# Optimization experiments

Hardware: AMD Instinct MI355X
Metric: run time of the kernel (lower is better)

Reference implementation:

```python
import jax, jax.numpy as jnp
import numpy as np

TOPK = 2


def setup_inputs() -> dict:
    key = jax.random.key(0)
    ks = jax.random.split(key, 6)
    B, S, D, H, M = 2, 2048, 256, 8, 8
    s = 0.02
    return {
        "x": jax.random.normal(ks[0], (B, S, D), jnp.float32),
        "Wq": jax.random.normal(ks[1], (D, H * D), jnp.float32) * s,
        "bq": jnp.zeros((H * D,), jnp.float32),
        "Wr": jax.random.normal(ks[2], (D, M), jnp.float32) * s,
        "br": jnp.zeros((M,), jnp.float32),
        "Wk": jax.random.normal(ks[3], (M, D, H * D), jnp.float32) * s,
        "bk": jnp.zeros((M, H * D), jnp.float32),
        "Wv": jax.random.normal(ks[4], (M, D, H * D), jnp.float32) * s,
        "bv": jnp.zeros((M, H * D), jnp.float32),
        "Wo": jax.random.normal(ks[5], (H * D, D), jnp.float32) * s,
        "bo": jnp.zeros((D,), jnp.float32),
        "bias0": jnp.zeros((B, M), jnp.float32),
    }


def reference(x, Wq, bq, Wr, br, Wk, bk, Wv, bv, Wo, bo, bias0):
    B, S, D = x.shape
    M, _, HD = Wk.shape
    H = HD // D
    # query projection and head split: [B,S,H,D] (head dim == n_text_state)
    q = (x @ Wq + bq).reshape(B, S, H, D)
    # router + aux-loss-free bias-adjusted top-k routing (DeepSeek-V3 style)
    scores = jax.nn.softmax(x @ Wr + br, axis=-1)                 # [B,S,M]
    biased = scores + bias0[:, None, :]
    _, idx = jax.lax.top_k(biased, TOPK)                          # [B,S,TOPK]
    mask = jax.nn.one_hot(idx, M, dtype=scores.dtype).sum(-2)     # [B,S,M] in {0,1}
    routing = scores * mask
    routing = routing / routing.sum(-1, keepdims=True)
    # per-memory linear-attention state: M_m = sum_s r[b,s,m] * k (x) v, fused over all memories
    k_all = (jnp.einsum('bsd,mde->mbse', x, Wk) + bk[:, None, None, :]).reshape(M, B, S, H, D)
    v_all = (jnp.einsum('bsd,mde->mbse', x, Wv) + bv[:, None, None, :]).reshape(M, B, S, H, D)
    mem = jnp.einsum('bsm,mbshk,mbshv->bhkv', routing, k_all, v_all)  # [B,H,D,D]
    # fused read-out (replaces per-timestep python loop): o[b,s,h,v] = sum_k mem[b,h,k,v] q[b,s,h,k]
    o = jnp.einsum('bhkv,bshk->bshv', mem, q)                     # [B,S,H,D]
    return o.reshape(B, S, H * D) @ Wo + bo
```

## Files before the change

kernel.cpp:

```cpp
#include <hip/hip_runtime.h>

typedef __attribute__((ext_vector_type(8))) short bf16x8;
typedef __attribute__((ext_vector_type(4))) float f32x4;

#define DEV static __device__ __forceinline__

DEV unsigned short f2bf(float f){
  union { float f; unsigned u; } v; v.f = f;
  unsigned r = v.u + 0x7fffu + ((v.u >> 16) & 1u);
  return (unsigned short)(r >> 16);
}
DEV float bf2f(unsigned short u){
  union { unsigned u; float f; } v; v.u = ((unsigned)u) << 16;
  return v.f;
}
DEV unsigned long long pk4(float a, float b, float c, float d){
  unsigned lo = (unsigned)f2bf(a) | ((unsigned)f2bf(b) << 16);
  unsigned hi = (unsigned)f2bf(c) | ((unsigned)f2bf(d) << 16);
  return ((unsigned long long)hi << 32) | lo;
}

__global__ __launch_bounds__(256) void k_prep(const float* __restrict__ x,
                                              const float* __restrict__ Wq,
                                              const float* __restrict__ Wr,
                                              const float* __restrict__ br,
                                              const float* __restrict__ Wk,
                                              const float* __restrict__ Wv,
                                              const float* __restrict__ Wo,
                                              const float* __restrict__ bias0,
                                              unsigned short* __restrict__ WkT,
                                              unsigned short* __restrict__ WvT,
                                              unsigned short* __restrict__ WoT,
                                              unsigned short* __restrict__ Wqb,
                                              unsigned short* __restrict__ xb,
                                              unsigned short* __restrict__ xT,
                                              float* __restrict__ routT){
  __shared__ float tile[32*33];
  __shared__ float lg[32][8];
  __shared__ float rt2[32][8];
  int bid = blockIdx.x;
  int t = threadIdx.x;
  int tx = t & 31, ty = t >> 5;

  if (bid < 8192){
    const float* src = (bid < 4096) ? Wk : Wv;
    unsigned short* dst = (bid < 4096) ? WkT : WvT;
    int q = bid & 4095;
    int bat = q >> 9, rem = q & 511;
    int c0 = (rem >> 3) * 32, r0 = (rem & 7) * 32;
    size_t boff = (size_t)bat * 256 * 2048;
    for (int i = 0; i < 4; i++)
      tile[(ty + i*8)*33 + tx] = src[boff + (size_t)(r0 + ty + i*8) * 2048 + c0 + tx];
    __syncthreads();
    for (int i = 0; i < 4; i++)
      dst[boff + (size_t)(c0 + ty + i*8) * 256 + r0 + tx] = f2bf(tile[tx*33 + ty + i*8]);
  } else if (bid < 8704){
    int q = bid - 8192;
    int c0 = (q >> 6) * 32, r0 = (q & 63) * 32;
    for (int i = 0; i < 4; i++)
      tile[(ty + i*8)*33 + tx] = Wo[(size_t)(r0 + ty + i*8) * 256 + c0 + tx];
    __syncthreads();
    for (int i = 0; i < 4; i++)
      WoT[(size_t)(c0 + ty + i*8) * 2048 + r0 + tx] = f2bf(tile[tx*33 + ty + i*8]);
  } else if (bid < 8960){
    int q = bid - 8704;
    size_t idx = (size_t)q * 2048 + t * 8;
    f32x4 a = *(const f32x4*)(Wq + idx);
    f32x4 b = *(const f32x4*)(Wq + idx + 4);
    *(unsigned long long*)(Wqb + idx)     = pk4(a[0], a[1], a[2], a[3]);
    *(unsigned long long*)(Wqb + idx + 4) = pk4(b[0], b[1], b[2], b[3]);
  } else if (bid < 9984){
    int q = bid - 8960;
    int bat = q >> 9, rem = q & 511;
    int c0 = (rem >> 6) * 32, r0 = (rem & 63) * 32;
    size_t boff = (size_t)bat * 2048 * 256;
    for (int i = 0; i < 4; i++){
      float v = x[boff + (size_t)(r0 + ty + i*8) * 256 + c0 + tx];
      tile[(ty + i*8)*33 + tx] = v;
      xb[boff + (size_t)(r0 + ty + i*8) * 256 + c0 + tx] = f2bf(v);
    }
    __syncthreads();
    for (int i = 0; i < 4; i++)
      xT[(size_t)(bat*256 + c0 + ty + i*8) * 2048 + r0 + tx] = f2bf(tile[tx*33 + ty + i*8]);
  } else {
    int row = t >> 3, mm = t & 7;
    int n = (bid - 9984) * 32 + row;
    const float* xr = x + (size_t)n * 256;
    float acc = 0.f;
    for (int d = 0; d < 256; d++) acc += xr[d] * Wr[d * 8 + mm];
    acc += br[mm];
    lg[row][mm] = acc;
    __syncthreads();
    if (t < 32){
      int r = t; int n2 = (bid - 9984) * 32 + r; int b = n2 >> 11;
      float mx = -1e30f;
      for (int i = 0; i < 8; i++) mx = fmaxf(mx, lg[r][i]);
      float s[8]; float sum = 0.f;
      for (int i = 0; i < 8; i++){ s[i] = __expf(lg[r][i] - mx); sum += s[i]; }
      for (int i = 0; i < 8; i++) s[i] /= sum;
      float bb[8];
      for (int i = 0; i < 8; i++) bb[i] = s[i] + bias0[b * 8 + i];
      int i1 = 0;
      for (int i = 1; i < 8; i++) if (bb[i] > bb[i1]) i1 = i;
      int i2 = -1;
      for (int i = 0; i < 8; i++){ if (i == i1) continue; if (i2 < 0 || bb[i] > bb[i2]) i2 = i; }
      float wsum = s[i1] + s[i2];
      for (int i = 0; i < 8; i++)
        rt2[r][i] = (i == i1) ? s[i1] / wsum : ((i == i2) ? s[i2] / wsum : 0.f);
    }
    __syncthreads();
    int n3 = (bid - 9984) * 32 + row;
    int b = n3 >> 11, sl = n3 & 2047;
    routT[((size_t)b * 8 + mm) * 2048 + sl] = rt2[row][mm];
  }
}

__global__ __launch_bounds__(256) void k_usum(const unsigned short* __restrict__ xb,
                                              const float* __restrict__ routT,
                                              float* __restrict__ upart, float* __restrict__ rhop){
  __shared__ float rl[128];
  int bid = blockIdx.x;
  int sc = bid & 15, bm = bid >> 4, b = bm >> 3;
  int t = threadIdx.x;
  int s0 = sc * 128;
  if (t < 128) rl[t] = routT[(size_t)bm * 2048 + s0 + t];
  __syncthreads();
  float acc = 0.f;
  const unsigned short* xrow = xb + ((size_t)(b * 2048 + s0)) * 256 + t;
  for (int s = 0; s < 128; s++){
    float rv = rl[s];
    if (rv != 0.f)
      acc += rv * bf2f(xrow[(size_t)s * 256]);
  }
  upart[(size_t)bid * 256 + t] = acc;
  if (t == 0){
    float rs = 0.f;
    for (int s = 0; s < 128; s++) rs += rl[s];
    rhop[bid] = rs;
  }
}

__global__ __launch_bounds__(256) void k_bias(const unsigned short* __restrict__ WkT,
                                              const unsigned short* __restrict__ WvT,
                                              const float* __restrict__ upart,
                                              const float* __restrict__ rhop,
                                              float* __restrict__ ku_g, float* __restrict__ vu_g,
                                              float* __restrict__ rho){
  __shared__ float uL[256];
  int bid = blockIdx.x, t = threadIdx.x;
  int bm = bid >> 3, hseg = bid & 7, m = bm & 7;
  {
    float s = 0.f;
    for (int scn = 0; scn < 16; scn++)
      s += upart[(size_t)(bm*16 + scn) * 256 + t];
    uL[t] = s;
  }
  if (hseg == 0 && t == 0){
    float rs = 0.f;
    for (int scn = 0; scn < 16; scn++) rs += rhop[bm*16 + scn];
    rho[bm] = rs;
  }
  __syncthreads();
  int hd = hseg * 256 + t;
  const unsigned short* wk = WkT + ((size_t)m*2048 + hd) * 256;
  const unsigned short* wv = WvT + ((size_t)m*2048 + hd) * 256;
  float sk = 0.f, sv = 0.f;
  for (int d8 = 0; d8 < 256; d8 += 8){
    bf16x8 a = *(const bf16x8*)(wk + d8);
    bf16x8 c = *(const bf16x8*)(wv + d8);
    for (int j = 0; j < 8; j++){
      sk += bf2f((unsigned short)a[j]) * uL[d8+j];
      sv += bf2f((unsigned short)c[j]) * uL[d8+j];
    }
  }
  ku_g[(size_t)bm*2048 + hd] = sk;
  vu_g[(size_t)bm*2048 + hd] = sv;
}

__global__ __launch_bounds__(512) void k_gpart(const unsigned short* __restrict__ xT,
                                               const float* __restrict__ routT,
                                               unsigned short* __restrict__ Gp){
  __shared__ unsigned short As[256*72];
  __shared__ unsigned short Bs[256*72];
  __shared__ float rl[64];
  int bid = blockIdx.x;
  int kc = bid & 7, m = (bid >> 3) & 7, b = bid >> 6;
  int bm = b * 8 + m;
  int t = threadIdx.x, lane = t & 63, w = t >> 6;
  int li = lane & 15, lgp = lane >> 4;
  int p = w >> 2, q = w & 3;
  f32x4 acc[8][4];
  for (int i = 0; i < 8; i++) for (int j = 0; j < 4; j++) acc[i][j] = (f32x4){0,0,0,0};
  for (int c4 = 0; c4 < 4; c4++){
    int s0 = kc * 256 + c4 * 64;
    if (t < 64) rl[t] = routT[(size_t)bm*2048 + s0 + t];
    __syncthreads();
    for (int qq = 0; qq < 4; qq++){
      int idx = t + qq*512;
      int row = idx >> 3, sc = (idx & 7) * 8;
      bf16x8 xv = *(const bf16x8*)(xT + ((size_t)(b*256 + row))*2048 + s0 + sc);
      *(bf16x8*)(&Bs[row*72 + sc]) = xv;
      f32x4 r0 = *(const f32x4*)(rl + sc);
      f32x4 r1 = *(const f32x4*)(rl + sc + 4);
      bf16x8 sv;
      sv[0]=(short)f2bf(bf2f((unsigned short)xv[0])*r0[0]);
      sv[1]=(short)f2bf(bf2f((unsigned short)xv[1])*r0[1]);
      sv[2]=(short)f2bf(bf2f((unsigned short)xv[2])*r0[2]);
      sv[3]=(short)f2bf(bf2f((unsigned short)xv[3])*r0[3]);
      sv[4]=(short)f2bf(bf2f((unsigned short)xv[4])*r1[0]);
      sv[5]=(short)f2bf(bf2f((unsigned short)xv[5])*r1[1]);
      sv[6]=(short)f2bf(bf2f((unsigned short)xv[6])*r1[2]);
      sv[7]=(short)f2bf(bf2f((unsigned short)xv[7])*r1[3]);
      *(bf16x8*)(&As[row*72 + sc]) = sv;
    }
    __syncthreads();
    for (int kk = 0; kk < 2; kk++){
      bf16x8 Bf[4];
      for (int j = 0; j < 4; j++)
        Bf[j] = *(const bf16x8*)(&Bs[(q*64 + j*16 + li)*72 + kk*32 + lgp*8]);
      for (int i = 0; i < 8; i++){
        bf16x8 Af = *(const bf16x8*)(&As[(p*128 + i*16 + li)*72 + kk*32 + lgp*8]);
        for (int j = 0; j < 4; j++)
          acc[i][j] = __builtin_amdgcn_mfma_f32_16x16x32_bf16(Af, Bf[j], acc[i][j], 0, 0, 0);
      }
    }
    __syncthreads();
  }
  unsigned short* Cs = As;
  for (int ph = 0; ph < 4; ph++){
    if (q == ph){
      for (int i = 0; i < 8; i++)
        for (int j = 0; j < 4; j++){
          int rr = j*16 + li, cc = p*128 + i*16 + lgp*4;
          *(unsigned long long*)(&Cs[rr*264 + cc]) =
            pk4(acc[i][j][0], acc[i][j][1], acc[i][j][2], acc[i][j][3]);
        }
    }
    __syncthreads();
    for (int qq = 0; qq < 4; qq++){
      int idx = t + qq*512;
      int row = idx >> 5, cc = (idx & 31) * 8;
      *(bf16x8*)(Gp + (((size_t)bm*8 + kc) << 16) + (size_t)(ph*64 + row)*256 + cc) =
        *(const bf16x8*)(&Cs[row*264 + cc]);
    }
    __syncthreads();
  }
}

__global__ __launch_bounds__(256) void k_gred(const unsigned short* __restrict__ Gp,
                                              unsigned short* __restrict__ G){
  int idx = blockIdx.x * 256 + threadIdx.x;
  int bm = idx >> 13; size_t e8 = (size_t)(idx & 8191) * 8;
  float s[8] = {0,0,0,0,0,0,0,0};
  for (int kc = 0; kc < 8; kc++){
    bf16x8 v = *(const bf16x8*)(Gp + (((size_t)bm*8 + kc) << 16) + e8);
    for (int j = 0; j < 8; j++) s[j] += bf2f((unsigned short)v[j]);
  }
  *(unsigned long long*)(G + ((size_t)bm << 16) + e8)     = pk4(s[0], s[1], s[2], s[3]);
  *(unsigned long long*)(G + ((size_t)bm << 16) + e8 + 4) = pk4(s[4], s[5], s[6], s[7]);
}

__global__ __launch_bounds__(512) void k_tmat(const unsigned short* __restrict__ G,
                                              const unsigned short* __restrict__ WvT,
                                              unsigned short* __restrict__ Tt){
  __shared__ unsigned short Cs[64*264];
  int bid = blockIdx.x;
  int hseg = bid & 15, bm = bid >> 4, m = bm & 7;
  int t = threadIdx.x, lane = t & 63, w = t >> 6;
  int li = lane & 15, lgp = lane >> 4;
  int r = w >> 1, c = w & 1;
  f32x4 acc[4][4];
  for (int i = 0; i < 4; i++) for (int j = 0; j < 4; j++) acc[i][j] = (f32x4){0,0,0,0};
  const unsigned short* gp = G + ((size_t)bm << 16) + (size_t)(r*64 + li)*256 + lgp*8;
  const unsigned short* wp = WvT + ((size_t)m*2048 + hseg*128 + c*64 + li)*256 + lgp*8;
  #pragma unroll
  for (int kk = 0; kk < 8; kk++){
    bf16x8 Bf[4];
    for (int j = 0; j < 4; j++)
      Bf[j] = *(const bf16x8*)(wp + (size_t)(j*16)*256 + kk*32);
    for (int i = 0; i < 4; i++){
      bf16x8 Af = *(const bf16x8*)(gp + (size_t)(i*16)*256 + kk*32);
      for (int j = 0; j < 4; j++)
        acc[i][j] = __builtin_amdgcn_mfma_f32_16x16x32_bf16(Af, Bf[j], acc[i][j], 0, 0, 0);
    }
  }
  for (int ph = 0; ph < 2; ph++){
    if (c == ph){
      for (int i = 0; i < 4; i++)
        for (int j = 0; j < 4; j++)
          *(unsigned long long*)(&Cs[(j*16 + li)*264 + r*64 + i*16 + lgp*4]) =
            pk4(acc[i][j][0], acc[i][j][1], acc[i][j][2], acc[i][j][3]);
    }
    __syncthreads();
    for (int q = 0; q < 4; q++){
      int idx = t + q*512;
      int row = idx >> 5, cc = (idx & 31) * 8;
      *(bf16x8*)(Tt + ((size_t)bm*2048 + hseg*128 + ph*64 + row)*256 + cc) =
        *(const bf16x8*)(&Cs[row*264 + cc]);
    }
    __syncthreads();
  }
}

__global__ __launch_bounds__(256) void k_kmat(const unsigned short* __restrict__ Tt,
                                              const unsigned short* __restrict__ WkT,
                                              const float* __restrict__ bk,
                                              const float* __restrict__ bv,
                                              const float* __restrict__ ku_g,
                                              const float* __restrict__ vu_g,
                                              const float* __restrict__ rho,
                                              unsigned short* __restrict__ memT){
  int bid = blockIdx.x;
  int kq = bid & 3, vq = (bid >> 2) & 3, bh = bid >> 4;
  int b = bh >> 3, h = bh & 7;
  int hd0 = h * 256;
  int t = threadIdx.x, lane = t & 63, w = t >> 6;
  int li = lane & 15, lgp = lane >> 4;
  int wr = w >> 1, wc = w & 1;
  f32x4 acc[2][2];
  for (int i = 0; i < 2; i++) for (int j = 0; j < 2; j++) acc[i][j] = (f32x4){0,0,0,0};
  #pragma unroll 2
  for (int m = 0; m < 8; m++){
    const unsigned short* ap = WkT + ((size_t)m*2048 + hd0 + kq*64 + wc*32 + li)*256 + lgp*8;
    const unsigned short* bp = Tt + ((size_t)(b*8 + m)*2048 + hd0 + vq*64 + wr*32 + li)*256 + lgp*8;
    #pragma unroll
    for (int kk = 0; kk < 8; kk++){
      bf16x8 Af[2], Bf[2];
      Af[0] = *(const bf16x8*)(ap + kk*32);
      Af[1] = *(const bf16x8*)(ap + 16*256 + kk*32);
      Bf[0] = *(const bf16x8*)(bp + kk*32);
      Bf[1] = *(const bf16x8*)(bp + 16*256 + kk*32);
      for (int i = 0; i < 2; i++)
        for (int j = 0; j < 2; j++)
          acc[i][j] = __builtin_amdgcn_mfma_f32_16x16x32_bf16(Af[i], Bf[j], acc[i][j], 0, 0, 0);
    }
  }
  float rhol[8];
  #pragma unroll
  for (int m = 0; m < 8; m++) rhol[m] = rho[b*8 + m];
  #pragma unroll
  for (int j = 0; j < 2; j++){
    int vdg = hd0 + vq*64 + wr*32 + j*16 + li;
    float bvv[8], bb[8];
    #pragma unroll
    for (int m = 0; m < 8; m++){
      bvv[m] = bv[(size_t)m*2048 + vdg];
      bb[m]  = vu_g[(size_t)(b*8+m)*2048 + vdg] + rhol[m]*bvv[m];
    }
    #pragma unroll
    for (int i = 0; i < 2; i++){
      int kdg = hd0 + kq*64 + wc*32 + i*16 + lgp*4;
      f32x4 s = acc[i][j];
      #pragma unroll
      for (int m = 0; m < 8; m++){
        f32x4 ku4 = *(const f32x4*)(ku_g + (size_t)(b*8+m)*2048 + kdg);
        f32x4 bk4 = *(const f32x4*)(bk + (size_t)m*2048 + kdg);
        s[0] += ku4[0]*bvv[m] + bk4[0]*bb[m];
        s[1] += ku4[1]*bvv[m] + bk4[1]*bb[m];
        s[2] += ku4[2]*bvv[m] + bk4[2]*bb[m];
        s[3] += ku4[3]*bvv[m] + bk4[3]*bb[m];
      }
      int vd = vq*64 + wr*32 + j*16 + li;
      int kd = kq*64 + wc*32 + i*16 + lgp*4;
      *(unsigned long long*)(memT + (size_t)bh*65536 + (size_t)vd*256 + kd) =
        pk4(s[0], s[1], s[2], s[3]);
    }
  }
}

__global__ __launch_bounds__(512) void k_emat(const unsigned short* __restrict__ memT,
                                              const unsigned short* __restrict__ Wqb,
                                              const float* __restrict__ bq,
                                              unsigned short* __restrict__ Eb,
                                              float* __restrict__ qbAll){
  __shared__ unsigned short Cs[16*264];
  int bid = blockIdx.x;
  int dseg = bid & 3, bh = bid >> 2;
  int b = bh >> 3, h = bh & 7;
  int hd0 = h * 256, d0 = dseg * 64;
  int t = threadIdx.x, lane = t & 63, w = t >> 6;
  int li = lane & 15, lgp = lane >> 4;
  int r = w >> 2, c = w & 3;
  f32x4 acc[8];
  for (int i = 0; i < 8; i++) acc[i] = (f32x4){0,0,0,0};
  for (int kk = 0; kk < 8; kk++){
    bf16x8 Bf = *(const bf16x8*)(Wqb + (size_t)(d0 + c*16 + li)*2048 + hd0 + kk*32 + lgp*8);
    for (int i = 0; i < 8; i++){
      bf16x8 Af = *(const bf16x8*)(memT + (size_t)bh*65536 + (size_t)(r*128 + i*16 + li)*256 + kk*32 + lgp*8);
      acc[i] = __builtin_amdgcn_mfma_f32_16x16x32_bf16(Af, Bf, acc[i], 0, 0, 0);
    }
  }
  if (dseg == 0 && t < 256){
    const unsigned short* mrow = memT + (size_t)bh*65536 + (size_t)t*256;
    float s = 0.f;
    for (int k8 = 0; k8 < 256; k8 += 8){
      bf16x8 v = *(const bf16x8*)(mrow + k8);
      for (int e = 0; e < 8; e++) s += bf2f((unsigned short)v[e]) * bq[hd0 + k8 + e];
    }
    qbAll[(size_t)b*2048 + hd0 + t] = s;
  }
  for (int ph = 0; ph < 4; ph++){
    if (c == ph){
      for (int i = 0; i < 8; i++)
        *(unsigned long long*)(&Cs[li*264 + r*128 + i*16 + lgp*4]) =
          pk4(acc[i][0], acc[i][1], acc[i][2], acc[i][3]);
    }
    __syncthreads();
    {
      int row = t >> 5, cc = (t & 31) * 8;
      *(bf16x8*)(Eb + (size_t)b*524288 + (size_t)(d0 + ph*16 + row)*2048 + hd0 + cc) =
        *(const bf16x8*)(&Cs[row*264 + cc]);
    }
    __syncthreads();
  }
}

__global__ __launch_bounds__(512) void k_fmat(const unsigned short* __restrict__ Eb,
                                              const unsigned short* __restrict__ WoT,
                                              const float* __restrict__ qbAll,
                                              const float* __restrict__ bo,
                                              float* __restrict__ Fpart,
                                              float* __restrict__ c0acc){
  __shared__ float qL[2048];
  int bid = blockIdx.x;
  int t = threadIdx.x;
  if (bid >= 256){
    int b = bid - 256;
    for (int i = t; i < 2048; i += 512) qL[i] = qbAll[(size_t)b * 2048 + i];
    __syncthreads();
    int w = t >> 6, lane = t & 63;
    for (int dd = w; dd < 256; dd += 8){
      const unsigned short* wrow = WoT + (size_t)dd * 2048 + lane * 8;
      const float* qp = qL + lane * 8;
      float s = 0.f;
      for (int pass = 0; pass < 4; pass++){
        bf16x8 v = *(const bf16x8*)(wrow + pass * 512);
        const float* q = qp + pass * 512;
        for (int e = 0; e < 8; e++) s += bf2f((unsigned short)v[e]) * q[e];
      }
      for (int off = 32; off; off >>= 1) s += __shfl_down(s, off);
      if (lane == 0) c0acc[(size_t)b * 256 + dd] = s + bo[dd];
    }
    return;
  }
  int ks = bid & 7, dseg = (bid >> 3) & 3, doseg = (bid >> 5) & 3, b = bid >> 7;
  int do0 = doseg * 64, d0 = dseg * 64, k0 = ks * 256;
  int lane = t & 63, w = t >> 6;
  int li = lane & 15, lgp = lane >> 4;
  int r = w >> 2, c = w & 3;
  f32x4 acc[2];
  acc[0] = (f32x4){0,0,0,0}; acc[1] = (f32x4){0,0,0,0};
  const unsigned short* bp = Eb + (size_t)b*524288 + (size_t)(d0 + c*16 + li)*2048 + k0 + lgp*8;
  const unsigned short* ap = WoT + (size_t)(do0 + r*32 + li)*2048 + k0 + lgp*8;
  #pragma unroll
  for (int kk = 0; kk < 8; kk++){
    bf16x8 Bf = *(const bf16x8*)(bp + kk*32);
    bf16x8 Af0 = *(const bf16x8*)(ap + kk*32);
    bf16x8 Af1 = *(const bf16x8*)(ap + kk*32 + 16*2048);
    acc[0] = __builtin_amdgcn_mfma_f32_16x16x32_bf16(Af0, Bf, acc[0], 0, 0, 0);
    acc[1] = __builtin_amdgcn_mfma_f32_16x16x32_bf16(Af1, Bf, acc[1], 0, 0, 0);
  }
  int dd = d0 + c*16 + li;
  float* Fp = Fpart + ((size_t)(ks*2 + b)) * 65536;
  for (int i = 0; i < 2; i++){
    int dor = do0 + r*32 + i*16 + lgp*4;
    float* p = Fp + (size_t)dor*256 + dd;
    p[0]   = acc[i][0];
    p[256] = acc[i][1];
    p[512] = acc[i][2];
    p[768] = acc[i][3];
  }
}

__global__ __launch_bounds__(256) void k_fred(const float* __restrict__ Fpart,
                                              unsigned short* __restrict__ Fb){
  int idx = blockIdx.x * 256 + threadIdx.x;
  int b = idx >> 14; int e4 = (idx & 16383) * 4;
  f32x4 s = (f32x4){0,0,0,0};
  for (int ks = 0; ks < 8; ks++){
    f32x4 v = *(const f32x4*)(Fpart + ((size_t)(ks*2 + b)) * 65536 + e4);
    s[0] += v[0]; s[1] += v[1]; s[2] += v[2]; s[3] += v[3];
  }
  *(unsigned long long*)(Fb + (size_t)b*65536 + e4) = pk4(s[0], s[1], s[2], s[3]);
}

__global__ __launch_bounds__(512) void k_final2(const unsigned short* __restrict__ Fb,
                                                const unsigned short* __restrict__ xb,
                                                const float* __restrict__ c0acc,
                                                float* __restrict__ out){
  int bid = blockIdx.x;
  int tc = bid & 31, b = bid >> 5;
  int t = threadIdx.x, lane = t & 63, w = t >> 6;
  int li = lane & 15, lgp = lane >> 4;
  int r = w >> 1, c = w & 1;
  int tok0 = b * 2048 + tc * 64;
  f32x4 acc[4][2];
  for (int i = 0; i < 4; i++) for (int j = 0; j < 2; j++) acc[i][j] = (f32x4){0,0,0,0};
  for (int kk = 0; kk < 8; kk++){
    bf16x8 Bf[2];
    for (int j = 0; j < 2; j++)
      Bf[j] = *(const bf16x8*)(xb + (size_t)(tok0 + c*32 + j*16 + li)*256 + kk*32 + lgp*8);
    for (int i = 0; i < 4; i++){
      bf16x8 af = *(const bf16x8*)(Fb + (size_t)b*65536 + (size_t)(r*64 + i*16 + li)*256 + kk*32 + lgp*8);
      for (int j = 0; j < 2; j++)
        acc[i][j] = __builtin_amdgcn_mfma_f32_16x16x32_bf16(af, Bf[j], acc[i][j], 0, 0, 0);
    }
  }
  for (int i = 0; i < 4; i++){
    int dol = r*64 + i*16 + lgp*4;
    f32x4 c4 = *(const f32x4*)(c0acc + (size_t)b*256 + dol);
    for (int j = 0; j < 2; j++){
      int tokl = c*32 + j*16 + li;
      f32x4 v = acc[i][j];
      v[0] += c4[0]; v[1] += c4[1]; v[2] += c4[2]; v[3] += c4[3];
      *(f32x4*)(out + (size_t)(tok0 + tokl)*256 + dol) = v;
    }
  }
}

extern "C" void kernel_launch(void* const* d_in, const int* in_sizes, int n_in,
                              void* d_out, int out_size, void* d_ws, size_t ws_size,
                              hipStream_t stream) {
  const float* x     = (const float*)d_in[0];
  const float* Wq    = (const float*)d_in[1];
  const float* bq    = (const float*)d_in[2];
  const float* Wr    = (const float*)d_in[3];
  const float* br    = (const float*)d_in[4];
  const float* Wk    = (const float*)d_in[5];
  const float* bk    = (const float*)d_in[6];
  const float* Wv    = (const float*)d_in[7];
  const float* bv    = (const float*)d_in[8];
  const float* Wo    = (const float*)d_in[9];
  const float* bo    = (const float*)d_in[10];
  const float* bias0 = (const float*)d_in[11];
  float* out = (float*)d_out;

  char* ws = (char*)d_ws;
  size_t off = 0;
  auto alloc = [&](size_t bytes) -> char* {
    char* p = ws + off;
    off = (off + bytes + 255) & ~(size_t)255;
    return p;
  };
  unsigned short* xb   = (unsigned short*)alloc((size_t)4096 * 256 * 2);
  unsigned short* xT   = (unsigned short*)alloc((size_t)2 * 256 * 2048 * 2);
  unsigned short* Wqb  = (unsigned short*)alloc((size_t)256 * 2048 * 2);
  unsigned short* WkT  = (unsigned short*)alloc((size_t)8 * 2048 * 256 * 2);
  unsigned short* WvT  = (unsigned short*)alloc((size_t)8 * 2048 * 256 * 2);
  unsigned short* WoT  = (unsigned short*)alloc((size_t)256 * 2048 * 2);
  float*          routT= (float*)alloc((size_t)16 * 2048 * 4);
  float*          upart= (float*)alloc((size_t)256 * 256 * 4);
  float*          rhop = (float*)alloc((size_t)256 * 4);
  float*          rho  = (float*)alloc((size_t)16 * 4);
  float*          ku_g = (float*)alloc((size_t)16 * 2048 * 4);
  float*          vu_g = (float*)alloc((size_t)16 * 2048 * 4);
  unsigned short* Gp   = (unsigned short*)alloc((size_t)16 * 8 * 65536 * 2);
  unsigned short* G    = (unsigned short*)alloc((size_t)16 * 65536 * 2);
  unsigned short* memT = (unsigned short*)alloc((size_t)16 * 65536 * 2);
  unsigned short* Eb   = (unsigned short*)alloc((size_t)2 * 256 * 2048 * 2);
  float*          qbAll= (float*)alloc((size_t)2 * 2048 * 4);
  float*          Fpart= (float*)alloc((size_t)16 * 65536 * 4);
  unsigned short* Fb   = (unsigned short*)alloc((size_t)2 * 65536 * 2);
  float*          c0acc= (float*)alloc((size_t)2 * 256 * 4);
  unsigned short* Tt   = Gp;
  (void)ws_size; (void)in_sizes; (void)n_in; (void)out_size;

  k_prep<<<10112, 256, 0, stream>>>(x, Wq, Wr, br, Wk, Wv, Wo, bias0,
                                    WkT, WvT, WoT, Wqb, xb, xT, routT);
  k_usum<<<256, 256, 0, stream>>>(xb, routT, upart, rhop);
  k_bias<<<128, 256, 0, stream>>>(WkT, WvT, upart, rhop, ku_g, vu_g, rho);
  k_gpart<<<128, 512, 0, stream>>>(xT, routT, Gp);
  k_gred<<<512, 256, 0, stream>>>(Gp, G);
  k_tmat<<<256, 512, 0, stream>>>(G, WvT, Tt);
  k_kmat<<<256, 256, 0, stream>>>(Tt, WkT, bk, bv, ku_g, vu_g, rho, memT);
  k_emat<<<64, 512, 0, stream>>>(memT, Wqb, bq, Eb, qbAll);
  k_fmat<<<258, 512, 0, stream>>>(Eb, WoT, qbAll, bo, Fpart, c0acc);
  k_fred<<<128, 256, 0, stream>>>(Fpart, Fb);
  k_final2<<<64, 512, 0, stream>>>(Fb, xb, c0acc, out);
}
```

Before: 208.0 us.

## Fuse T-matrix and K-matrix stages into one kernel with reassociated product

Replaces the separate k_tmat (G·Wv per head segment, written to global Tt) and k_kmat (WkT·Tt summed over memories) kernels with a single k_mem2 kernel. It first computes Wk-slice·G into shared memory and then multiplies that by Wv, accumulating over the 8 memories. This reassociates the product so each block handles a 32-row k slice over the full v range, and the Tt intermediate never goes to global memory. It removes one launch and the global round-trip of Tt. In exchange it uses fewer blocks (128), adds per-memory syncthreads, and rounds an extra intermediate to bf16 in shared memory.

After: 246.2 us. +18.4%, slower.

```diff
diff --git a/kernel.cpp b/kernel.cpp
--- a/kernel.cpp
+++ b/kernel.cpp
@@ -260,87 +260,70 @@
   *(unsigned long long*)(G + ((size_t)bm << 16) + e8 + 4) = pk4(s[4], s[5], s[6], s[7]);
 }
 
-__global__ __launch_bounds__(512) void k_tmat(const unsigned short* __restrict__ G,
+__global__ __launch_bounds__(512) void k_mem2(const unsigned short* __restrict__ G,
+                                              const unsigned short* __restrict__ WkT,
                                               const unsigned short* __restrict__ WvT,
-                                              unsigned short* __restrict__ Tt){
-  __shared__ unsigned short Cs[64*264];
-  int bid = blockIdx.x;
-  int hseg = bid & 15, bm = bid >> 4, m = bm & 7;
-  int t = threadIdx.x, lane = t & 63, w = t >> 6;
-  int li = lane & 15, lgp = lane >> 4;
-  int r = w >> 1, c = w & 1;
-  f32x4 acc[4][4];
-  for (int i = 0; i < 4; i++) for (int j = 0; j < 4; j++) acc[i][j] = (f32x4){0,0,0,0};
-  const unsigned short* gp = G + ((size_t)bm << 16) + (size_t)(r*64 + li)*256 + lgp*8;
-  const unsigned short* wp = WvT + ((size_t)m*2048 + hseg*128 + c*64 + li)*256 + lgp*8;
-  #pragma unroll
-  for (int kk = 0; kk < 8; kk++){
-    bf16x8 Bf[4];
-    for (int j = 0; j < 4; j++)
-      Bf[j] = *(const bf16x8*)(wp + (size_t)(j*16)*256 + kk*32);
-    for (int i = 0; i < 4; i++){
-      bf16x8 Af = *(const bf16x8*)(gp + (size_t)(i*16)*256 + kk*32);
-      for (int j = 0; j < 4; j++)
-        acc[i][j] = __builtin_amdgcn_mfma_f32_16x16x32_bf16(Af, Bf[j], acc[i][j], 0, 0, 0);
-    }
-  }
-  for (int ph = 0; ph < 2; ph++){
-    if (c == ph){
-      for (int i = 0; i < 4; i++)
-        for (int j = 0; j < 4; j++)
-          *(unsigned long long*)(&Cs[(j*16 + li)*264 + r*64 + i*16 + lgp*4]) =
-            pk4(acc[i][j][0], acc[i][j][1], acc[i][j][2], acc[i][j][3]);
-    }
-    __syncthreads();
-    for (int q = 0; q < 4; q++){
-      int idx = t + q*512;
-      int row = idx >> 5, cc = (idx & 31) * 8;
-      *(bf16x8*)(Tt + ((size_t)bm*2048 + hseg*128 + ph*64 + row)*256 + cc) =
-        *(const bf16x8*)(&Cs[row*264 + cc]);
-    }
-    __syncthreads();
-  }
-}
-
-__global__ __launch_bounds__(256) void k_kmat(const unsigned short* __restrict__ Tt,
-                                              const unsigned short* __restrict__ WkT,
                                               const float* __restrict__ bk,
                                               const float* __restrict__ bv,
                                               const float* __restrict__ ku_g,
                                               const float* __restrict__ vu_g,
                                               const float* __restrict__ rho,
                                               unsigned short* __restrict__ memT){
-  int bid = blockIdx.x;
-  int kq = bid & 3, vq = (bid >> 2) & 3, bh = bid >> 4;
+  __shared__ unsigned short Y[32*280];
+  int lb = blockIdx.x;
+  int bid = (lb & 7) * 16 + (lb >> 3);
+  int kq = bid & 7, bh = bid >> 3;
   int b = bh >> 3, h = bh & 7;
-  int hd0 = h * 256;
+  int hd0 = h * 256, kd0 = kq * 32;
   int t = threadIdx.x, lane = t & 63, w = t >> 6;
   int li = lane & 15, lgp = lane >> 4;
-  int wr = w >> 1, wc = w & 1;
-  f32x4 acc[2][2];
-  for (int i = 0; i < 2; i++) for (int j = 0; j < 2; j++) acc[i][j] = (f32x4){0,0,0,0};
-  #pragma unroll 2
+
+  f32x4 acc2[2][2];
+  for (int i = 0; i < 2; i++) for (int j = 0; j < 2; j++) acc2[i][j] = (f32x4){0,0,0,0};
+
   for (int m = 0; m < 8; m++){
-    const unsigned short* ap = WkT + ((size_t)m*2048 + hd0 + kq*64 + wc*32 + li)*256 + lgp*8;
-    const unsigned short* bp = Tt + ((size_t)(b*8 + m)*2048 + hd0 + vq*64 + wr*32 + li)*256 + lgp*8;
+    int bm = b * 8 + m;
+    f32x4 a1[2][2];
+    for (int i = 0; i < 2; i++) for (int j = 0; j < 2; j++) a1[i][j] = (f32x4){0,0,0,0};
+    const unsigned short* gp  = G + ((size_t)bm << 16) + (size_t)(w*32 + li)*256 + lgp*8;
+    const unsigned short* wkp = WkT + ((size_t)m*2048 + hd0 + kd0 + li)*256 + lgp*8;
     #pragma unroll
     for (int kk = 0; kk < 8; kk++){
-      bf16x8 Af[2], Bf[2];
-      Af[0] = *(const bf16x8*)(ap + kk*32);
-      Af[1] = *(const bf16x8*)(ap + 16*256 + kk*32);
-      Bf[0] = *(const bf16x8*)(bp + kk*32);
-      Bf[1] = *(const bf16x8*)(bp + 16*256 + kk*32);
-      for (int i = 0; i < 2; i++)
-        for (int j = 0; j < 2; j++)
-          acc[i][j] = __builtin_amdgcn_mfma_f32_16x16x32_bf16(Af[i], Bf[j], acc[i][j], 0, 0, 0);
-    }
+      bf16x8 Ag[2], Bk[2];
+      Ag[0] = *(const bf16x8*)(gp + kk*32);
+      Ag[1] = *(const bf16x8*)(gp + 16*256 + kk*32);
+      Bk[0] = *(const bf16x8*)(wkp + kk*32);
+      Bk[1] = *(const bf16x8*)(wkp + 16*256 + kk*32);
+      for (int bi = 0; bi < 2; bi++)
+        for (int ai = 0; ai < 2; ai++)
+          a1[bi][ai] = __builtin_amdgcn_mfma_f32_16x16x32_bf16(Ag[ai], Bk[bi], a1[bi][ai], 0, 0, 0);
+    }
+    for (int bi = 0; bi < 2; bi++)
+      for (int ai = 0; ai < 2; ai++)
+        *(unsigned long long*)(&Y[(bi*16 + li)*280 + w*32 + ai*16 + lgp*4]) =
+          pk4(a1[bi][ai][0], a1[bi][ai][1], a1[bi][ai][2], a1[bi][ai][3]);
+    __syncthreads();
+    const unsigned short* wvp = WvT + ((size_t)m*2048 + hd0 + w*32 + li)*256 + lgp*8;
+    #pragma unroll
+    for (int kk = 0; kk < 8; kk++){
+      bf16x8 Ay[2], Bv[2];
+      Ay[0] = *(const bf16x8*)(&Y[(li)*280 + kk*32 + lgp*8]);
+      Ay[1] = *(const bf16x8*)(&Y[(16 + li)*280 + kk*32 + lgp*8]);
+      Bv[0] = *(const bf16x8*)(wvp + kk*32);
+      Bv[1] = *(const bf16x8*)(wvp + 16*256 + kk*32);
+      for (int ai2 = 0; ai2 < 2; ai2++)
+        for (int bj = 0; bj < 2; bj++)
+          acc2[ai2][bj] = __builtin_amdgcn_mfma_f32_16x16x32_bf16(Ay[ai2], Bv[bj], acc2[ai2][bj], 0, 0, 0);
+    }
+    __syncthreads();
   }
   float rhol[8];
   #pragma unroll
   for (int m = 0; m < 8; m++) rhol[m] = rho[b*8 + m];
   #pragma unroll
-  for (int j = 0; j < 2; j++){
-    int vdg = hd0 + vq*64 + wr*32 + j*16 + li;
+  for (int bj = 0; bj < 2; bj++){
+    int vd = w*32 + bj*16 + li;
+    int vdg = hd0 + vd;
     float bvv[8], bb[8];
     #pragma unroll
     for (int m = 0; m < 8; m++){
@@ -348,9 +331,10 @@
       bb[m]  = vu_g[(size_t)(b*8+m)*2048 + vdg] + rhol[m]*bvv[m];
     }
     #pragma unroll
-    for (int i = 0; i < 2; i++){
-      int kdg = hd0 + kq*64 + wc*32 + i*16 + lgp*4;
-      f32x4 s = acc[i][j];
+    for (int ai2 = 0; ai2 < 2; ai2++){
+      int kd = kd0 + ai2*16 + lgp*4;
+      int kdg = hd0 + kd;
+      f32x4 s = acc2[ai2][bj];
       #pragma unroll
       for (int m = 0; m < 8; m++){
         f32x4 ku4 = *(const f32x4*)(ku_g + (size_t)(b*8+m)*2048 + kdg);
@@ -360,8 +344,6 @@
         s[2] += ku4[2]*bvv[m] + bk4[2]*bb[m];
         s[3] += ku4[3]*bvv[m] + bk4[3]*bb[m];
       }
-      int vd = vq*64 + wr*32 + j*16 + li;
-      int kd = kq*64 + wc*32 + i*16 + lgp*4;
       *(unsigned long long*)(memT + (size_t)bh*65536 + (size_t)vd*256 + kd) =
         pk4(s[0], s[1], s[2], s[3]);
     }
@@ -562,7 +544,6 @@
   float*          Fpart= (float*)alloc((size_t)16 * 65536 * 4);
   unsigned short* Fb   = (unsigned short*)alloc((size_t)2 * 65536 * 2);
   float*          c0acc= (float*)alloc((size_t)2 * 256 * 4);
-  unsigned short* Tt   = Gp;
   (void)ws_size; (void)in_sizes; (void)n_in; (void)out_size;
 
   k_prep<<<10112, 256, 0, stream>>>(x, Wq, Wr, br, Wk, Wv, Wo, bias0,
@@ -571,8 +552,7 @@
   k_bias<<<128, 256, 0, stream>>>(WkT, WvT, upart, rhop, ku_g, vu_g, rho);
   k_gpart<<<128, 512, 0, stream>>>(xT, routT, Gp);
   k_gred<<<512, 256, 0, stream>>>(Gp, G);
-  k_tmat<<<256, 512, 0, stream>>>(G, WvT, Tt);
-  k_kmat<<<256, 256, 0, stream>>>(Tt, WkT, bk, bv, ku_g, vu_g, rho, memT);
+  k_mem2<<<128, 512, 0, stream>>>(G, WkT, WvT, bk, bv, ku_g, vu_g, rho, memT);
   k_emat<<<64, 512, 0, stream>>>(memT, Wqb, bq, Eb, qbAll);
   k_fmat<<<258, 512, 0, stream>>>(Eb, WoT, qbAll, bo, Fpart, c0acc);
   k_fred<<<128, 256, 0, stream>>>(Fpart, Fb);
```

## Split k_kmat over memories into partial GEMM plus separate reduction kernel

Applied to the files above, without the earlier changes.

The per-(b,h) memory-state GEMM, which looped over 8 memories inside each block, is split so each block handles one memory. Partial fp32 results go to a new 32 MB workspace, and a new reduction kernel sums them and applies the bias corrections before packing to bf16. This raises grid parallelism from 256 to 512 larger blocks and drops the serial m-loop. In exchange it adds a kernel launch and substantial global-memory traffic for the partials.

Result: no change. 208.2 us (+0.1%).

```diff
diff --git a/kernel.cpp b/kernel.cpp
--- a/kernel.cpp
+++ b/kernel.cpp
@@ -302,70 +302,75 @@
   }
 }
 
-__global__ __launch_bounds__(256) void k_kmat(const unsigned short* __restrict__ Tt,
-                                              const unsigned short* __restrict__ WkT,
+__global__ __launch_bounds__(512) void k_kmat3(const unsigned short* __restrict__ Tt,
+                                               const unsigned short* __restrict__ WkT,
+                                               float* __restrict__ mempartF){
+  int bid = blockIdx.x;
+  int m = bid & 7, kq = (bid >> 3) & 1, vq = (bid >> 4) & 1, bh = bid >> 5;
+  int b = bh >> 3, h = bh & 7;
+  int hd0 = h * 256;
+  int t = threadIdx.x, lane = t & 63, w = t >> 6;
+  int li = lane & 15, lgp = lane >> 4;
+  int wr = w >> 2, wc = w & 3;
+  f32x4 acc[2][4];
+  for (int i = 0; i < 2; i++) for (int j = 0; j < 4; j++) acc[i][j] = (f32x4){0,0,0,0};
+  const unsigned short* ap = WkT + ((size_t)m*2048 + hd0 + kq*128 + wc*32 + li)*256 + lgp*8;
+  const unsigned short* bp = Tt + ((size_t)(b*8 + m)*2048 + hd0 + vq*128 + wr*64 + li)*256 + lgp*8;
+  #pragma unroll
+  for (int kk = 0; kk < 8; kk++){
+    bf16x8 Af[2], Bf[4];
+    Af[0] = *(const bf16x8*)(ap + kk*32);
+    Af[1] = *(const bf16x8*)(ap + 16*256 + kk*32);
+    for (int j = 0; j < 4; j++)
+      Bf[j] = *(const bf16x8*)(bp + (size_t)(j*16)*256 + kk*32);
+    for (int i = 0; i < 2; i++)
+      for (int j = 0; j < 4; j++)
+        acc[i][j] = __builtin_amdgcn_mfma_f32_16x16x32_bf16(Af[i], Bf[j], acc[i][j], 0, 0, 0);
+  }
+  float* Fp = mempartF + ((((size_t)(m*16 + bh))*2 + vq)*2 + kq) * 16384;
+  for (int j = 0; j < 4; j++){
+    int vdt = wr*64 + j*16 + li;
+    for (int i = 0; i < 2; i++){
+      int kdt = wc*32 + i*16 + lgp*4;
+      *(f32x4*)(Fp + (size_t)vdt*128 + kdt) = acc[i][j];
+    }
+  }
+}
+
+__global__ __launch_bounds__(256) void k_kred(const float* __restrict__ mempartF,
                                               const float* __restrict__ bk,
                                               const float* __restrict__ bv,
                                               const float* __restrict__ ku_g,
                                               const float* __restrict__ vu_g,
                                               const float* __restrict__ rho,
                                               unsigned short* __restrict__ memT){
-  int bid = blockIdx.x;
-  int kq = bid & 3, vq = (bid >> 2) & 3, bh = bid >> 4;
+  int idx = blockIdx.x * 256 + threadIdx.x;
+  int bh = idx >> 14;
+  int rem = idx & 16383;
+  int vd = rem >> 6, kd = (rem & 63) * 4;
   int b = bh >> 3, h = bh & 7;
-  int hd0 = h * 256;
-  int t = threadIdx.x, lane = t & 63, w = t >> 6;
-  int li = lane & 15, lgp = lane >> 4;
-  int wr = w >> 1, wc = w & 1;
-  f32x4 acc[2][2];
-  for (int i = 0; i < 2; i++) for (int j = 0; j < 2; j++) acc[i][j] = (f32x4){0,0,0,0};
-  #pragma unroll 2
+  int vdg = h*256 + vd, kdg = h*256 + kd;
+  int vq = vd >> 7, kq = kd >> 7;
+  size_t src = ((((size_t)bh)*2 + vq)*2 + kq) * 16384 + (size_t)(vd & 127)*128 + (kd & 127);
+  f32x4 s = (f32x4){0,0,0,0};
+  #pragma unroll
   for (int m = 0; m < 8; m++){
-    const unsigned short* ap = WkT + ((size_t)m*2048 + hd0 + kq*64 + wc*32 + li)*256 + lgp*8;
-    const unsigned short* bp = Tt + ((size_t)(b*8 + m)*2048 + hd0 + vq*64 + wr*32 + li)*256 + lgp*8;
-    #pragma unroll
-    for (int kk = 0; kk < 8; kk++){
-      bf16x8 Af[2], Bf[2];
-      Af[0] = *(const bf16x8*)(ap + kk*32);
-      Af[1] = *(const bf16x8*)(ap + 16*256 + kk*32);
-      Bf[0] = *(const bf16x8*)(bp + kk*32);
-      Bf[1] = *(const bf16x8*)(bp + 16*256 + kk*32);
-      for (int i = 0; i < 2; i++)
-        for (int j = 0; j < 2; j++)
-          acc[i][j] = __builtin_amdgcn_mfma_f32_16x16x32_bf16(Af[i], Bf[j], acc[i][j], 0, 0, 0);
-    }
-  }
-  float rhol[8];
+    f32x4 v = *(const f32x4*)(mempartF + (size_t)m*16*65536 + src);
+    s[0] += v[0]; s[1] += v[1]; s[2] += v[2]; s[3] += v[3];
+  }
   #pragma unroll
-  for (int m = 0; m < 8; m++) rhol[m] = rho[b*8 + m];
-  #pragma unroll
-  for (int j = 0; j < 2; j++){
-    int vdg = hd0 + vq*64 + wr*32 + j*16 + li;
-    float bvv[8], bb[8];
-    #pragma unroll
-    for (int m = 0; m < 8; m++){
-      bvv[m] = bv[(size_t)m*2048 + vdg];
-      bb[m]  = vu_g[(size_t)(b*8+m)*2048 + vdg] + rhol[m]*bvv[m];
-    }
-    #pragma unroll
-    for (int i = 0; i < 2; i++){
-      int kdg = hd0 + kq*64 + wc*32 + i*16 + lgp*4;
-      f32x4 s = acc[i][j];
-      #pragma unroll
-      for (int m = 0; m < 8; m++){
-        f32x4 ku4 = *(const f32x4*)(ku_g + (size_t)(b*8+m)*2048 + kdg);
-        f32x4 bk4 = *(const f32x4*)(bk + (size_t)m*2048 + kdg);
-        s[0] += ku4[0]*bvv[m] + bk4[0]*bb[m];
-        s[1] += ku4[1]*bvv[m] + bk4[1]*bb[m];
-        s[2] += ku4[2]*bvv[m] + bk4[2]*bb[m];
-        s[3] += ku4[3]*bvv[m] + bk4[3]*bb[m];
-      }
-      int vd = vq*64 + wr*32 + j*16 + li;
-      int kd = kq*64 + wc*32 + i*16 + lgp*4;
-      *(unsigned long long*)(memT + (size_t)bh*65536 + (size_t)vd*256 + kd) =
-        pk4(s[0], s[1], s[2], s[3]);
-    }
-  }
+  for (int m = 0; m < 8; m++){
+    float bvv = bv[(size_t)m*2048 + vdg];
+    float bb  = vu_g[(size_t)(b*8+m)*2048 + vdg] + rho[b*8+m]*bvv;
+    f32x4 ku4 = *(const f32x4*)(ku_g + (size_t)(b*8+m)*2048 + kdg);
+    f32x4 bk4 = *(const f32x4*)(bk + (size_t)m*2048 + kdg);
+    s[0] += ku4[0]*bvv + bk4[0]*bb;
+    s[1] += ku4[1]*bvv + bk4[1]*bb;
+    s[2] += ku4[2]*bvv + bk4[2]*bb;
+    s[3] += ku4[3]*bvv + bk4[3]*bb;
+  }
+  *(unsigned long long*)(memT + (size_t)bh*65536 + (size_t)vd*256 + kd) =
+    pk4(s[0], s[1], s[2], s[3]);
 }
 
 __global__ __launch_bounds__(512) void k_emat(const unsigned short* __restrict__ memT,
@@ -562,6 +567,7 @@
   float*          Fpart= (float*)alloc((size_t)16 * 65536 * 4);
   unsigned short* Fb   = (unsigned short*)alloc((size_t)2 * 65536 * 2);
   float*          c0acc= (float*)alloc((size_t)2 * 256 * 4);
+  float*          mempartF = (float*)alloc((size_t)8 * 16 * 65536 * 4);
   unsigned short* Tt   = Gp;
   (void)ws_size; (void)in_sizes; (void)n_in; (void)out_size;
 
@@ -572,7 +578,8 @@
   k_gpart<<<128, 512, 0, stream>>>(xT, routT, Gp);
   k_gred<<<512, 256, 0, stream>>>(Gp, G);
   k_tmat<<<256, 512, 0, stream>>>(G, WvT, Tt);
-  k_kmat<<<256, 256, 0, stream>>>(Tt, WkT, bk, bv, ku_g, vu_g, rho, memT);
+  k_kmat3<<<512, 512, 0, stream>>>(Tt, WkT, mempartF);
+  k_kred<<<1024, 256, 0, stream>>>(mempartF, bk, bv, ku_g, vu_g, rho, memT);
   k_emat<<<64, 512, 0, stream>>>(memT, Wqb, bq, Eb, qbAll);
   k_fmat<<<258, 512, 0, stream>>>(Eb, WoT, qbAll, bo, Fpart, c0acc);
   k_fred<<<128, 256, 0, stream>>>(Fpart, Fb);
```
